# Kernel tuning notes

Measured on AMD Instinct MI355X. Metric: run time of the kernel, lower is better.

The kernel has to match this reference:

```python
import jax, jax.numpy as jnp
import numpy as np

N_NODES = 100000
N_EDGES = 1600000
VOCAB = 10000
HIDDEN = 128
EMB1 = 128
EMB2 = 128
L1 = 64
N_GRAPHS = 256


def setup_inputs() -> dict:
    key = jax.random.key(0)
    ks = jax.random.split(key, 16)
    inp = {
        "x": jax.random.randint(ks[0], (N_NODES,), 0, VOCAB, dtype=jnp.int32),
        "edge_index": jax.random.randint(ks[1], (2, N_EDGES), 0, N_NODES, dtype=jnp.int32),
        "edge_weight": jax.random.uniform(ks[2], (N_EDGES,), dtype=jnp.float32),
        "batch": jnp.sort(jax.random.randint(ks[3], (N_NODES,), 0, N_GRAPHS, dtype=jnp.int32)),
        # parameters
        "emb_w": jax.random.normal(ks[4], (VOCAB, HIDDEN), dtype=jnp.float32) * 0.5,
        "w1_rel": jax.random.normal(ks[5], (EMB1, HIDDEN), dtype=jnp.float32) * (HIDDEN ** -0.5),
        "b1_rel": jnp.zeros((EMB1,), dtype=jnp.float32),
        "w1_root": jax.random.normal(ks[6], (EMB1, HIDDEN), dtype=jnp.float32) * (HIDDEN ** -0.5),
        "w2_rel": jax.random.normal(ks[7], (EMB2, EMB1), dtype=jnp.float32) * (EMB1 ** -0.5),
        "b2_rel": jnp.zeros((EMB2,), dtype=jnp.float32),
        "w2_root": jax.random.normal(ks[8], (EMB2, EMB1), dtype=jnp.float32) * (EMB1 ** -0.5),
        "cls1_w": jax.random.normal(ks[9], (L1, EMB2), dtype=jnp.float32) * (EMB2 ** -0.5),
        "cls1_b": jnp.zeros((L1,), dtype=jnp.float32),
        "cls2_w": jax.random.normal(ks[10], (2, L1), dtype=jnp.float32) * (L1 ** -0.5),
        "cls2_b": jnp.zeros((2,), dtype=jnp.float32),
    }
    return inp


def _embedding_max_norm(emb_w, idx, max_norm=1.0):
    # torch Embedding(max_norm=1): looked-up rows are renormalized to norm <= 1
    rows = emb_w[idx]                                        # [N, H]
    norm = jnp.linalg.norm(rows, axis=-1, keepdims=True)
    scale = jnp.minimum(1.0, max_norm / (norm + 1e-7))
    return rows * scale


def _graph_conv(h, src, dst, ew, w_rel, b_rel, w_root):
    # PyG GraphConv: out = lin_rel(sum_{j->i} w_ji * x_j) + lin_root(x_i)
    msg = h[src] * ew[:, None]                               # [E, D] gather
    agg = jax.ops.segment_sum(msg, dst, num_segments=N_NODES)  # [N, D] scatter-add
    return agg @ w_rel.T + b_rel + h @ w_root.T


def reference(x, edge_index, edge_weight, batch, emb_w,
              w1_rel, b1_rel, w1_root, w2_rel, b2_rel, w2_root,
              cls1_w, cls1_b, cls2_w, cls2_b):
    src, dst = edge_index[0], edge_index[1]
    h = _embedding_max_norm(emb_w, x)                        # [N, HIDDEN]
    # dropout is identity in eval mode
    h = jax.nn.relu(_graph_conv(h, src, dst, edge_weight, w1_rel, b1_rel, w1_root))
    h = jax.nn.relu(_graph_conv(h, src, dst, edge_weight, w2_rel, b2_rel, w2_root))
    # global mean pool over graphs
    sums = jax.ops.segment_sum(h, batch, num_segments=N_GRAPHS)        # [G, EMB2]
    counts = jax.ops.segment_sum(jnp.ones((h.shape[0],), h.dtype), batch,
                                 num_segments=N_GRAPHS)
    pooled = sums / jnp.maximum(counts, 1.0)[:, None]
    z = jax.nn.relu(pooled @ cls1_w.T + cls1_b)
    z = z @ cls2_w.T + cls2_b
    return jax.nn.softmax(z, axis=1)                          # [G, 2]
```

## Files before the change

kernel.cpp:

```cpp
#include <hip/hip_runtime.h>
#include <stdint.h>

#define NN 100000
#define NE 1600000
#define NG 256
#define NB 196
#define CHUNK 4096
#define NCH 391
#define NGS 392

typedef __attribute__((ext_vector_type(8))) short bf16x8;
typedef __attribute__((ext_vector_type(4))) float f32x4;

__device__ inline uint32_t f2bf(float f){
    uint32_t u = __float_as_uint(f);
    return (u + 0x7FFFu + ((u >> 16) & 1u)) >> 16;
}
__device__ inline float bflo(uint32_t u){ return __uint_as_float(u << 16); }
__device__ inline float bfhi(uint32_t u){ return __uint_as_float(u & 0xFFFF0000u); }
__device__ inline float bf1(short s){ return __uint_as_float(((uint32_t)(uint16_t)s) << 16); }

__global__ __launch_bounds__(256) void k_pack(const float* __restrict__ w1rel, const float* __restrict__ w1root,
                                              const float* __restrict__ w2rel, const float* __restrict__ w2root,
                                              short* __restrict__ wf, int* __restrict__ bcnt){
    int id = blockIdx.x * 256 + threadIdx.x;
    if (id < NB) bcnt[id] = 0;
    int i = id & 7, lane = (id >> 3) & 63, ks = (id >> 9) & 3, j0 = (id >> 11) & 7, m = id >> 14;
    const float* W = (m == 0) ? w1rel : (m == 1) ? w1root : (m == 2) ? w2rel : w2root;
    int j = j0 * 16 + (lane & 15);
    int k = ks * 32 + (lane >> 4) * 8 + i;
    wf[id] = (short)f2bf(W[j * 128 + k]);
}

__global__ __launch_bounds__(256) void k_embed(const int* __restrict__ x,
                                               const float* __restrict__ emb,
                                               uint32_t* __restrict__ hout,
                                               const int* __restrict__ edst,
                                               int* __restrict__ bcnt,
                                               const int* __restrict__ batch,
                                               int* __restrict__ gstart){
    int bid = blockIdx.x;
    if (bid < NN / 4){
        int w = threadIdx.x >> 6, l = threadIdx.x & 63;
        int n = bid * 4 + w;
        int r = x[n];
        const float2* e2 = (const float2*)emb;
        float2 v = e2[(size_t)r * 64 + l];
        float ss = v.x * v.x + v.y * v.y;
        #pragma unroll
        for (int off = 32; off; off >>= 1) ss += __shfl_xor(ss, off, 64);
        float sc = fminf(1.f, 1.f / (sqrtf(ss) + 1e-7f));
        hout[(size_t)n * 64 + l] = f2bf(v.x * sc) | (f2bf(v.y * sc) << 16);
    } else if (bid < NN / 4 + NCH){
        __shared__ int lh[NB];
        int t = threadIdx.x;
        int c0 = (bid - NN / 4) * CHUNK;
        int cnt = min(CHUNK, NE - c0);
        if (t < NB) lh[t] = 0;
        __syncthreads();
        for (int i = t; i < cnt; i += 256) atomicAdd(&lh[edst[c0 + i] >> 9], 1);
        __syncthreads();
        if (t < NB && lh[t]) atomicAdd(&bcnt[t], lh[t]);
    } else {
        int i = (bid - NN / 4 - NCH) * 256 + threadIdx.x;
        if (i > NN) return;
        int bprev = (i == 0) ? -1 : batch[i - 1];
        int bcur  = (i == NN) ? NG : batch[i];
        for (int g = bprev + 1; g <= bcur; ++g) gstart[g] = i;
    }
}

__global__ __launch_bounds__(256) void k_bscan(const int* __restrict__ bcnt,
                                               int* __restrict__ bbase, int* __restrict__ bfill,
                                               int* __restrict__ ptrA){
    __shared__ int sc[256];
    int t = threadIdx.x;
    int v = (t < NB) ? bcnt[t] : 0;
    sc[t] = v; __syncthreads();
    for (int off = 1; off < 256; off <<= 1){
        int u = (t >= off) ? sc[t - off] : 0;
        __syncthreads();
        sc[t] += u;
        __syncthreads();
    }
    if (t < NB){ bbase[t] = sc[t] - v; bfill[t] = 0; }
    if (t == 0){ bbase[NB] = NE; ptrA[NN] = NE; }
}

__global__ __launch_bounds__(256) void k_bscatter(const int* __restrict__ esrc, const int* __restrict__ edst,
                                                  const float* __restrict__ ew,
                                                  const int* __restrict__ bbase, int* __restrict__ bfill,
                                                  uint2* __restrict__ cse2){
    __shared__ uint2 rec[CHUNK];
    __shared__ unsigned char slotb[CHUNK];
    __shared__ int hist[NB], start[NB], gbase[NB], sc[256];
    int t = threadIdx.x;
    int c0 = blockIdx.x * CHUNK;
    int cnt = min(CHUNK, NE - c0);
    if (t < NB) hist[t] = 0;
    __syncthreads();
    for (int i = t; i < cnt; i += 256) atomicAdd(&hist[edst[c0 + i] >> 9], 1);
    __syncthreads();
    int v = (t < NB) ? hist[t] : 0;
    sc[t] = v; __syncthreads();
    for (int off = 1; off < 256; off <<= 1){
        int u = (t >= off) ? sc[t - off] : 0;
        __syncthreads();
        sc[t] += u;
        __syncthreads();
    }
    if (t < NB){
        start[t] = sc[t] - v;
        if (v > 0) gbase[t] = bbase[t] + atomicAdd(&bfill[t], v);
    }
    __syncthreads();
    if (t < NB) hist[t] = 0;
    __syncthreads();
    for (int i = t; i < cnt; i += 256){
        int d = edst[c0 + i];
        int b = d >> 9;
        int slot = start[b] + atomicAdd(&hist[b], 1);
        rec[slot] = make_uint2((uint32_t)esrc[c0 + i] | ((uint32_t)(d & 511) << 23),
                               __float_as_uint(ew[c0 + i]));
        slotb[slot] = (unsigned char)b;
    }
    __syncthreads();
    for (int i = t; i < cnt; i += 256){
        int b = slotb[i];
        cse2[gbase[b] + (i - start[b])] = rec[i];
    }
}

__global__ __launch_bounds__(256) void k_bcsr(const uint2* __restrict__ cse2,
                                              const int* __restrict__ bbase,
                                              int* __restrict__ ptrA,
                                              uint2* __restrict__ cse){
    __shared__ int cnt[512], sc[512], st[512];
    int t = threadIdx.x;
    int b = blockIdx.x;
    int ebase = bbase[b], eend = bbase[b + 1];
    int nb = b << 9;
    cnt[t] = 0; cnt[t + 256] = 0;
    __syncthreads();
    for (int i = ebase + t; i < eend; i += 256){
        uint2 r = cse2[i];
        atomicAdd(&cnt[r.x >> 23], 1);
    }
    __syncthreads();
    sc[t] = cnt[t]; sc[t + 256] = cnt[t + 256];
    __syncthreads();
    for (int off = 1; off < 512; off <<= 1){
        int v0 = (t >= off) ? sc[t - off] : 0;
        int v1 = sc[t + 256 - off];
        __syncthreads();
        sc[t] += v0; sc[t + 256] += v1;
        __syncthreads();
    }
    st[t] = sc[t] - cnt[t];
    st[t + 256] = sc[t + 256] - cnt[t + 256];
    if (nb + t < NN)       ptrA[nb + t]       = ebase + st[t];
    if (nb + 256 + t < NN) ptrA[nb + 256 + t] = ebase + st[t + 256];
    cnt[t] = 0; cnt[t + 256] = 0;
    __syncthreads();
    for (int i = ebase + t; i < eend; i += 256){
        uint2 r = cse2[i];
        int dr = r.x >> 23;
        int pos = st[dr] + atomicAdd(&cnt[dr], 1);
        cse[ebase + pos] = make_uint2(r.x & 0x7FFFFFu, r.y);
    }
}

__global__ __launch_bounds__(256) void k_agg(const uint32_t* __restrict__ hin,
                                             uint32_t* __restrict__ aggo,
                                             const int* __restrict__ ptr,
                                             const uint2* __restrict__ cse){
    int w = threadIdx.x >> 6, l = threadIdx.x & 63;
    int h = l >> 5, c = l & 31;
    int n = blockIdx.x * 4 + w;
    int p0 = ptr[n], p1 = ptr[n + 1];
    const uint2* hin2 = (const uint2*)hin;
    float a0 = 0, a1 = 0, a2 = 0, a3 = 0;
    float b0 = 0, b1 = 0, b2 = 0, b3 = 0;
    int e = p0;
    for (; e + 8 <= p1; e += 8){
        uint2 rA0 = cse[e + 2 * h],     rB0 = cse[e + 2 * h + 1];
        uint2 rA1 = cse[e + 4 + 2 * h], rB1 = cse[e + 4 + 2 * h + 1];
        uint2 vA0 = hin2[(size_t)rA0.x * 32 + c];
        uint2 vB0 = hin2[(size_t)rB0.x * 32 + c];
        uint2 vA1 = hin2[(size_t)rA1.x * 32 + c];
        uint2 vB1 = hin2[(size_t)rB1.x * 32 + c];
        float wA0 = __uint_as_float(rA0.y), wB0 = __uint_as_float(rB0.y);
        float wA1 = __uint_as_float(rA1.y), wB1 = __uint_as_float(rB1.y);
        a0 += wA0 * bflo(vA0.x); a1 += wA0 * bfhi(vA0.x);
        a2 += wA0 * bflo(vA0.y); a3 += wA0 * bfhi(vA0.y);
        b0 += wB0 * bflo(vB0.x); b1 += wB0 * bfhi(vB0.x);
        b2 += wB0 * bflo(vB0.y); b3 += wB0 * bfhi(vB0.y);
        a0 += wA1 * bflo(vA1.x); a1 += wA1 * bfhi(vA1.x);
        a2 += wA1 * bflo(vA1.y); a3 += wA1 * bfhi(vA1.y);
        b0 += wB1 * bflo(vB1.x); b1 += wB1 * bfhi(vB1.x);
        b2 += wB1 * bflo(vB1.y); b3 += wB1 * bfhi(vB1.y);
    }
    for (; e + 4 <= p1; e += 4){
        uint2 rA = cse[e + 2 * h], rB = cse[e + 2 * h + 1];
        uint2 vA = hin2[(size_t)rA.x * 32 + c];
        uint2 vB = hin2[(size_t)rB.x * 32 + c];
        float wA = __uint_as_float(rA.y), wB = __uint_as_float(rB.y);
        a0 += wA * bflo(vA.x); a1 += wA * bfhi(vA.x);
        a2 += wA * bflo(vA.y); a3 += wA * bfhi(vA.y);
        b0 += wB * bflo(vB.x); b1 += wB * bfhi(vB.x);
        b2 += wB * bflo(vB.y); b3 += wB * bfhi(vB.y);
    }
    for (; e < p1; e += 2){
        int idx = e + h;
        bool act = idx < p1;
        uint2 r = act ? cse[idx] : make_uint2(0u, 0u);
        uint2 v = hin2[(size_t)r.x * 32 + c];
        float wt = act ? __uint_as_float(r.y) : 0.f;
        a0 += wt * bflo(v.x); a1 += wt * bfhi(v.x);
        a2 += wt * bflo(v.y); a3 += wt * bfhi(v.y);
    }
    a0 += b0; a1 += b1; a2 += b2; a3 += b3;
    a0 += __shfl_xor(a0, 32, 64);
    a1 += __shfl_xor(a1, 32, 64);
    a2 += __shfl_xor(a2, 32, 64);
    a3 += __shfl_xor(a3, 32, 64);
    if (h == 0){
        uint2 o;
        o.x = f2bf(a0) | (f2bf(a1) << 16);
        o.y = f2bf(a2) | (f2bf(a3) << 16);
        ((uint2*)aggo)[(size_t)n * 32 + c] = o;
    }
}

__global__ __launch_bounds__(256) void k_gemm(const short* __restrict__ hin,
                                              const short* __restrict__ agg,
                                              short* __restrict__ hout,
                                              const bf16x8* __restrict__ wrel,
                                              const bf16x8* __restrict__ wroot,
                                              const float* __restrict__ bias){
    int t = threadIdx.x, w = t >> 6, l = t & 63;
    int rbase = blockIdx.x * 128 + w * 32;
    int r0 = rbase + (l & 15);
    int rA0 = min(r0, NN - 1);
    int rA1 = min(r0 + 16, NN - 1);
    int kb = (l >> 4) * 8;

    bf16x8 aA[2][4], aH[2][4];
    const short* pa0 = agg + (size_t)rA0 * 128 + kb;
    const short* pa1 = agg + (size_t)rA1 * 128 + kb;
    const short* ph0 = hin + (size_t)rA0 * 128 + kb;
    const short* ph1 = hin + (size_t)rA1 * 128 + kb;
    #pragma unroll
    for (int ks = 0; ks < 4; ++ks){
        aA[0][ks] = *(const bf16x8*)(pa0 + ks * 32);
        aA[1][ks] = *(const bf16x8*)(pa1 + ks * 32);
        aH[0][ks] = *(const bf16x8*)(ph0 + ks * 32);
        aH[1][ks] = *(const bf16x8*)(ph1 + ks * 32);
    }

    for (int j0 = 0; j0 < 8; ++j0){
        f32x4 acc0 = {0.f, 0.f, 0.f, 0.f}, acc1 = {0.f, 0.f, 0.f, 0.f};
        #pragma unroll
        for (int ks = 0; ks < 4; ++ks){
            bf16x8 br = wrel [(j0 * 4 + ks) * 64 + l];
            bf16x8 bo = wroot[(j0 * 4 + ks) * 64 + l];
            acc0 = __builtin_amdgcn_mfma_f32_16x16x32_bf16(aA[0][ks], br, acc0, 0, 0, 0);
            acc0 = __builtin_amdgcn_mfma_f32_16x16x32_bf16(aH[0][ks], bo, acc0, 0, 0, 0);
            acc1 = __builtin_amdgcn_mfma_f32_16x16x32_bf16(aA[1][ks], br, acc1, 0, 0, 0);
            acc1 = __builtin_amdgcn_mfma_f32_16x16x32_bf16(aH[1][ks], bo, acc1, 0, 0, 0);
        }
        int col = j0 * 16 + (l & 15);
        float bv = bias[col];
        int rb = rbase + (l >> 4) * 4;
        #pragma unroll
        for (int r = 0; r < 4; ++r){
            int row = rb + r;
            if (row < NN){
                float v = fmaxf(acc0[r] + bv, 0.f);
                hout[(size_t)row * 128 + col] = (short)f2bf(v);
            }
            int row1 = rb + 16 + r;
            if (row1 < NN){
                float v = fmaxf(acc1[r] + bv, 0.f);
                hout[(size_t)row1 * 128 + col] = (short)f2bf(v);
            }
        }
    }
}

__global__ __launch_bounds__(128) void k_poolcls(const short* __restrict__ h,
                                                 const int* __restrict__ gstart,
                                                 const float* __restrict__ c1w, const float* __restrict__ c1b,
                                                 const float* __restrict__ c2w, const float* __restrict__ c2b,
                                                 float* __restrict__ out){
    __shared__ float pl[128];
    __shared__ float z[64];
    __shared__ float logits[2];
    int g = blockIdx.x, t = threadIdx.x;
    int s = gstart[g], e = gstart[g + 1];
    float a0 = 0, a1 = 0, a2 = 0, a3 = 0;
    int i = s;
    for (; i + 3 < e; i += 4){
        a0 += bf1(h[(size_t)i * 128 + t]);
        a1 += bf1(h[(size_t)(i + 1) * 128 + t]);
        a2 += bf1(h[(size_t)(i + 2) * 128 + t]);
        a3 += bf1(h[(size_t)(i + 3) * 128 + t]);
    }
    for (; i < e; ++i) a0 += bf1(h[(size_t)i * 128 + t]);
    float sum = (a0 + a1) + (a2 + a3);
    int cnt = e - s;
    pl[t] = sum / fmaxf((float)cnt, 1.f);
    __syncthreads();
    if (t < 64){
        float acc = c1b[t];
        #pragma unroll 4
        for (int k = 0; k < 128; ++k) acc += pl[k] * c1w[t * 128 + k];
        z[t] = fmaxf(acc, 0.f);
    }
    __syncthreads();
    if (t < 2){
        float a = c2b[t];
        for (int k = 0; k < 64; ++k) a += z[k] * c2w[t * 64 + k];
        logits[t] = a;
    }
    __syncthreads();
    if (t == 0){
        float m = fmaxf(logits[0], logits[1]);
        float e0 = expf(logits[0] - m), e1 = expf(logits[1] - m);
        float ss = e0 + e1;
        out[g * 2 + 0] = e0 / ss;
        out[g * 2 + 1] = e1 / ss;
    }
}

extern "C" void kernel_launch(void* const* d_in, const int* in_sizes, int n_in,
                              void* d_out, int out_size, void* d_ws, size_t ws_size,
                              hipStream_t stream) {
    const int*   x      = (const int*)  d_in[0];
    const int*   eidx   = (const int*)  d_in[1];
    const float* ew     = (const float*)d_in[2];
    const int*   batch  = (const int*)  d_in[3];
    const float* emb    = (const float*)d_in[4];
    const float* w1rel  = (const float*)d_in[5];
    const float* b1     = (const float*)d_in[6];
    const float* w1root = (const float*)d_in[7];
    const float* w2rel  = (const float*)d_in[8];
    const float* b2     = (const float*)d_in[9];
    const float* w2root = (const float*)d_in[10];
    const float* c1w    = (const float*)d_in[11];
    const float* c1b    = (const float*)d_in[12];
    const float* c2w    = (const float*)d_in[13];
    const float* c2b    = (const float*)d_in[14];
    float* out = (float*)d_out;

    const int N = NN;
    const int E = NE;

    char* p = (char*)d_ws;
    auto alloc = [&](size_t bytes) -> void* {
        void* r = (void*)p;
        p += (bytes + 255) & ~(size_t)255;
        return r;
    };
    uint32_t* hA   = (uint32_t*)alloc((size_t)N * 64 * 4);
    uint32_t* hB   = (uint32_t*)alloc((size_t)N * 64 * 4);
    uint32_t* agg  = (uint32_t*)alloc((size_t)N * 64 * 4);
    int*   ptrA   = (int*)  alloc((size_t)(N + 1) * 4);
    int*   bcnt   = (int*)  alloc(NB * 4);
    int*   bbase  = (int*)  alloc((NB + 1) * 4);
    int*   bfill  = (int*)  alloc(NB * 4);
    uint2* cse2   = (uint2*)alloc((size_t)E * 8);
    uint2* cse    = (uint2*)alloc((size_t)E * 8);
    int*   gstart = (int*)  alloc((NG + 1) * 4);
    short* wf     = (short*)alloc(4 * 16384 * 2);
    (void)alloc(65536);

    const bf16x8* wf1rel  = (const bf16x8*)(wf);
    const bf16x8* wf1root = (const bf16x8*)(wf + 16384);
    const bf16x8* wf2rel  = (const bf16x8*)(wf + 32768);
    const bf16x8* wf2root = (const bf16x8*)(wf + 49152);

    const int* esrc = eidx;
    const int* edst = eidx + E;

    k_pack <<<256, 256, 0, stream>>>(w1rel, w1root, w2rel, w2root, wf, bcnt);
    k_embed<<<N / 4 + NCH + NGS, 256, 0, stream>>>(x, emb, hA, edst, bcnt, batch, gstart);

    k_bscan   <<<1,   256, 0, stream>>>(bcnt, bbase, bfill, ptrA);
    k_bscatter<<<NCH, 256, 0, stream>>>(esrc, edst, ew, bbase, bfill, cse2);
    k_bcsr    <<<NB,  256, 0, stream>>>(cse2, bbase, ptrA, cse);

    int ngemm = (N + 127) / 128;
    k_agg <<<N / 4, 256, 0, stream>>>(hA, agg, ptrA, cse);
    k_gemm<<<ngemm, 256, 0, stream>>>((const short*)hA, (const short*)agg, (short*)hB,
                                      wf1rel, wf1root, b1);
    k_agg <<<N / 4, 256, 0, stream>>>(hB, agg, ptrA, cse);
    k_gemm<<<ngemm, 256, 0, stream>>>((const short*)hB, (const short*)agg, (short*)hA,
                                      wf2rel, wf2root, b2);

    k_poolcls<<<NG, 128, 0, stream>>>((const short*)hA, gstart, c1w, c1b, c2w, c2b, out);
}
```

Baseline: 377.0 us.

## Use 16-byte gathers with quarter-wave edges and finer dst buckets

The aggregation kernel now has 16 lanes per 256-byte row, each loading a uint4 (8 bf16 values), and 4 edges in flight per wave instead of 2. CSR entries store the precomputed byte offset of the source row, so address math is a single add. Destination buckets shrink from 512 to 256 nodes (391 buckets), which changes the packing bits and the per-bucket local sort. This raises bytes per gather instruction and memory-level parallelism, in exchange for a larger bucket histogram and a two-step 8-accumulator shuffle reduction.

```diff
diff --git a/kernel.cpp b/kernel.cpp
--- a/kernel.cpp
+++ b/kernel.cpp
@@ -4,7 +4,7 @@
 #define NN 100000
 #define NE 1600000
 #define NG 256
-#define NB 196
+#define NB 391
 #define CHUNK 4096
 #define NCH 391
 #define NGS 392
@@ -56,11 +56,13 @@
         int t = threadIdx.x;
         int c0 = (bid - NN / 4) * CHUNK;
         int cnt = min(CHUNK, NE - c0);
-        if (t < NB) lh[t] = 0;
-        __syncthreads();
-        for (int i = t; i < cnt; i += 256) atomicAdd(&lh[edst[c0 + i] >> 9], 1);
-        __syncthreads();
-        if (t < NB && lh[t]) atomicAdd(&bcnt[t], lh[t]);
+        lh[t] = 0;
+        if (t + 256 < NB) lh[t + 256] = 0;
+        __syncthreads();
+        for (int i = t; i < cnt; i += 256) atomicAdd(&lh[edst[c0 + i] >> 8], 1);
+        __syncthreads();
+        if (lh[t]) atomicAdd(&bcnt[t], lh[t]);
+        if (t + 256 < NB && lh[t + 256]) atomicAdd(&bcnt[t + 256], lh[t + 256]);
     } else {
         int i = (bid - NN / 4 - NCH) * 256 + threadIdx.x;
         if (i > NN) return;
@@ -73,17 +75,21 @@
 __global__ __launch_bounds__(256) void k_bscan(const int* __restrict__ bcnt,
                                                int* __restrict__ bbase, int* __restrict__ bfill,
                                                int* __restrict__ ptrA){
-    __shared__ int sc[256];
+    __shared__ int sc[512];
     int t = threadIdx.x;
-    int v = (t < NB) ? bcnt[t] : 0;
-    sc[t] = v; __syncthreads();
-    for (int off = 1; off < 256; off <<= 1){
-        int u = (t >= off) ? sc[t - off] : 0;
-        __syncthreads();
-        sc[t] += u;
-        __syncthreads();
-    }
-    if (t < NB){ bbase[t] = sc[t] - v; bfill[t] = 0; }
+    int v0 = (t < NB) ? bcnt[t] : 0;
+    int v1 = (t + 256 < NB) ? bcnt[t + 256] : 0;
+    sc[t] = v0; sc[t + 256] = v1;
+    __syncthreads();
+    for (int off = 1; off < 512; off <<= 1){
+        int u0 = (t >= off) ? sc[t - off] : 0;
+        int u1 = sc[t + 256 - off];
+        __syncthreads();
+        sc[t] += u0; sc[t + 256] += u1;
+        __syncthreads();
+    }
+    if (t < NB){ bbase[t] = sc[t] - v0; bfill[t] = 0; }
+    if (t + 256 < NB){ bbase[t + 256] = sc[t + 256] - v1; bfill[t + 256] = 0; }
     if (t == 0){ bbase[NB] = NE; ptrA[NN] = NE; }
 }
 
@@ -92,37 +98,39 @@
                                                   const int* __restrict__ bbase, int* __restrict__ bfill,
                                                   uint2* __restrict__ cse2){
     __shared__ uint2 rec[CHUNK];
-    __shared__ unsigned char slotb[CHUNK];
-    __shared__ int hist[NB], start[NB], gbase[NB], sc[256];
+    __shared__ unsigned short slotb[CHUNK];
+    __shared__ int hist[512], start[512], gbase[512], sc[512];
     int t = threadIdx.x;
     int c0 = blockIdx.x * CHUNK;
     int cnt = min(CHUNK, NE - c0);
-    if (t < NB) hist[t] = 0;
-    __syncthreads();
-    for (int i = t; i < cnt; i += 256) atomicAdd(&hist[edst[c0 + i] >> 9], 1);
-    __syncthreads();
-    int v = (t < NB) ? hist[t] : 0;
-    sc[t] = v; __syncthreads();
-    for (int off = 1; off < 256; off <<= 1){
-        int u = (t >= off) ? sc[t - off] : 0;
-        __syncthreads();
-        sc[t] += u;
-        __syncthreads();
-    }
-    if (t < NB){
-        start[t] = sc[t] - v;
-        if (v > 0) gbase[t] = bbase[t] + atomicAdd(&bfill[t], v);
-    }
-    __syncthreads();
-    if (t < NB) hist[t] = 0;
+    hist[t] = 0; hist[t + 256] = 0;
+    __syncthreads();
+    for (int i = t; i < cnt; i += 256) atomicAdd(&hist[edst[c0 + i] >> 8], 1);
+    __syncthreads();
+    int v0 = hist[t], v1 = hist[t + 256];
+    sc[t] = v0; sc[t + 256] = v1;
+    __syncthreads();
+    for (int off = 1; off < 512; off <<= 1){
+        int u0 = (t >= off) ? sc[t - off] : 0;
+        int u1 = sc[t + 256 - off];
+        __syncthreads();
+        sc[t] += u0; sc[t + 256] += u1;
+        __syncthreads();
+    }
+    start[t] = sc[t] - v0;
+    start[t + 256] = sc[t + 256] - v1;
+    if (t < NB && v0 > 0) gbase[t] = bbase[t] + atomicAdd(&bfill[t], v0);
+    if (t + 256 < NB && v1 > 0) gbase[t + 256] = bbase[t + 256] + atomicAdd(&bfill[t + 256], v1);
+    __syncthreads();
+    hist[t] = 0; hist[t + 256] = 0;
     __syncthreads();
     for (int i = t; i < cnt; i += 256){
         int d = edst[c0 + i];
-        int b = d >> 9;
+        int b = d >> 8;
         int slot = start[b] + atomicAdd(&hist[b], 1);
-        rec[slot] = make_uint2((uint32_t)esrc[c0 + i] | ((uint32_t)(d & 511) << 23),
+        rec[slot] = make_uint2((uint32_t)esrc[c0 + i] | ((uint32_t)(d & 255) << 20),
                                __float_as_uint(ew[c0 + i]));
-        slotb[slot] = (unsigned char)b;
+        slotb[slot] = (unsigned short)b;
     }
     __syncthreads();
     for (int i = t; i < cnt; i += 256){
@@ -135,100 +143,102 @@
                                               const int* __restrict__ bbase,
                                               int* __restrict__ ptrA,
                                               uint2* __restrict__ cse){
-    __shared__ int cnt[512], sc[512], st[512];
+    __shared__ int cnt[256], sc[256], st[256];
     int t = threadIdx.x;
     int b = blockIdx.x;
     int ebase = bbase[b], eend = bbase[b + 1];
-    int nb = b << 9;
-    cnt[t] = 0; cnt[t + 256] = 0;
+    int nb = b << 8;
+    cnt[t] = 0;
+    __syncthreads();
+    for (int i = ebase + t; i < eend; i += 256){
+        atomicAdd(&cnt[cse2[i].x >> 20], 1);
+    }
+    __syncthreads();
+    int v = cnt[t];
+    sc[t] = v;
+    __syncthreads();
+    for (int off = 1; off < 256; off <<= 1){
+        int u = (t >= off) ? sc[t - off] : 0;
+        __syncthreads();
+        sc[t] += u;
+        __syncthreads();
+    }
+    st[t] = sc[t] - v;
+    if (nb + t < NN) ptrA[nb + t] = ebase + st[t];
+    cnt[t] = 0;
     __syncthreads();
     for (int i = ebase + t; i < eend; i += 256){
         uint2 r = cse2[i];
-        atomicAdd(&cnt[r.x >> 23], 1);
-    }
-    __syncthreads();
-    sc[t] = cnt[t]; sc[t + 256] = cnt[t + 256];
-    __syncthreads();
-    for (int off = 1; off < 512; off <<= 1){
-        int v0 = (t >= off) ? sc[t - off] : 0;
-        int v1 = sc[t + 256 - off];
-        __syncthreads();
-        sc[t] += v0; sc[t + 256] += v1;
-        __syncthreads();
-    }
-    st[t] = sc[t] - cnt[t];
-    st[t + 256] = sc[t + 256] - cnt[t + 256];
-    if (nb + t < NN)       ptrA[nb + t]       = ebase + st[t];
-    if (nb + 256 + t < NN) ptrA[nb + 256 + t] = ebase + st[t + 256];
-    cnt[t] = 0; cnt[t + 256] = 0;
-    __syncthreads();
-    for (int i = ebase + t; i < eend; i += 256){
-        uint2 r = cse2[i];
-        int dr = r.x >> 23;
+        int dr = r.x >> 20;
         int pos = st[dr] + atomicAdd(&cnt[dr], 1);
-        cse[ebase + pos] = make_uint2(r.x & 0x7FFFFFu, r.y);
-    }
-}
+        cse[ebase + pos] = make_uint2((r.x & 0xFFFFFu) << 8, r.y);
+    }
+}
+
+#define ACC8(vv, ww) \
+    a0 += ww * bflo(vv.x); a1 += ww * bfhi(vv.x); \
+    a2 += ww * bflo(vv.y); a3 += ww * bfhi(vv.y); \
+    a4 += ww * bflo(vv.z); a5 += ww * bfhi(vv.z); \
+    a6 += ww * bflo(vv.w); a7 += ww * bfhi(vv.w);
 
 __global__ __launch_bounds__(256) void k_agg(const uint32_t* __restrict__ hin,
                                              uint32_t* __restrict__ aggo,
                                              const int* __restrict__ ptr,
                                              const uint2* __restrict__ cse){
     int w = threadIdx.x >> 6, l = threadIdx.x & 63;
-    int h = l >> 5, c = l & 31;
+    int q = l >> 4, c = l & 15;
     int n = blockIdx.x * 4 + w;
     int p0 = ptr[n], p1 = ptr[n + 1];
-    const uint2* hin2 = (const uint2*)hin;
-    float a0 = 0, a1 = 0, a2 = 0, a3 = 0;
-    float b0 = 0, b1 = 0, b2 = 0, b3 = 0;
+    const char* hb = (const char*)hin;
+    uint32_t coff = (uint32_t)(c << 4);
+    float a0 = 0, a1 = 0, a2 = 0, a3 = 0, a4 = 0, a5 = 0, a6 = 0, a7 = 0;
     int e = p0;
+    for (; e + 16 <= p1; e += 16){
+        uint2 r0 = cse[e + q], r1 = cse[e + 4 + q], r2 = cse[e + 8 + q], r3 = cse[e + 12 + q];
+        uint4 v0 = *(const uint4*)(hb + (r0.x + coff));
+        uint4 v1 = *(const uint4*)(hb + (r1.x + coff));
+        uint4 v2 = *(const uint4*)(hb + (r2.x + coff));
+        uint4 v3 = *(const uint4*)(hb + (r3.x + coff));
+        float w0 = __uint_as_float(r0.y), w1 = __uint_as_float(r1.y);
+        float w2 = __uint_as_float(r2.y), w3 = __uint_as_float(r3.y);
+        ACC8(v0, w0); ACC8(v1, w1); ACC8(v2, w2); ACC8(v3, w3);
+    }
     for (; e + 8 <= p1; e += 8){
-        uint2 rA0 = cse[e + 2 * h],     rB0 = cse[e + 2 * h + 1];
-        uint2 rA1 = cse[e + 4 + 2 * h], rB1 = cse[e + 4 + 2 * h + 1];
-        uint2 vA0 = hin2[(size_t)rA0.x * 32 + c];
-        uint2 vB0 = hin2[(size_t)rB0.x * 32 + c];
-        uint2 vA1 = hin2[(size_t)rA1.x * 32 + c];
-        uint2 vB1 = hin2[(size_t)rB1.x * 32 + c];
-        float wA0 = __uint_as_float(rA0.y), wB0 = __uint_as_float(rB0.y);
-        float wA1 = __uint_as_float(rA1.y), wB1 = __uint_as_float(rB1.y);
-        a0 += wA0 * bflo(vA0.x); a1 += wA0 * bfhi(vA0.x);
-        a2 += wA0 * bflo(vA0.y); a3 += wA0 * bfhi(vA0.y);
-        b0 += wB0 * bflo(vB0.x); b1 += wB0 * bfhi(vB0.x);
-        b2 += wB0 * bflo(vB0.y); b3 += wB0 * bfhi(vB0.y);
-        a0 += wA1 * bflo(vA1.x); a1 += wA1 * bfhi(vA1.x);
-        a2 += wA1 * bflo(vA1.y); a3 += wA1 * bfhi(vA1.y);
-        b0 += wB1 * bflo(vB1.x); b1 += wB1 * bfhi(vB1.x);
-        b2 += wB1 * bflo(vB1.y); b3 += wB1 * bfhi(vB1.y);
+        uint2 r0 = cse[e + q], r1 = cse[e + 4 + q];
+        uint4 v0 = *(const uint4*)(hb + (r0.x + coff));
+        uint4 v1 = *(const uint4*)(hb + (r1.x + coff));
+        float w0 = __uint_as_float(r0.y), w1 = __uint_as_float(r1.y);
+        ACC8(v0, w0); ACC8(v1, w1);
     }
     for (; e + 4 <= p1; e += 4){
-        uint2 rA = cse[e + 2 * h], rB = cse[e + 2 * h + 1];
-        uint2 vA = hin2[(size_t)rA.x * 32 + c];
-        uint2 vB = hin2[(size_t)rB.x * 32 + c];
-        float wA = __uint_as_float(rA.y), wB = __uint_as_float(rB.y);
-        a0 += wA * bflo(vA.x); a1 += wA * bfhi(vA.x);
-        a2 += wA * bflo(vA.y); a3 += wA * bfhi(vA.y);
-        b0 += wB * bflo(vB.x); b1 += wB * bfhi(vB.x);
-        b2 += wB * bflo(vB.y); b3 += wB * bfhi(vB.y);
-    }
-    for (; e < p1; e += 2){
-        int idx = e + h;
-        bool act = idx < p1;
-        uint2 r = act ? cse[idx] : make_uint2(0u, 0u);
-        uint2 v = hin2[(size_t)r.x * 32 + c];
-        float wt = act ? __uint_as_float(r.y) : 0.f;
-        a0 += wt * bflo(v.x); a1 += wt * bfhi(v.x);
-        a2 += wt * bflo(v.y); a3 += wt * bfhi(v.y);
-    }
-    a0 += b0; a1 += b1; a2 += b2; a3 += b3;
-    a0 += __shfl_xor(a0, 32, 64);
-    a1 += __shfl_xor(a1, 32, 64);
-    a2 += __shfl_xor(a2, 32, 64);
-    a3 += __shfl_xor(a3, 32, 64);
-    if (h == 0){
-        uint2 o;
+        uint2 r0 = cse[e + q];
+        uint4 v0 = *(const uint4*)(hb + (r0.x + coff));
+        float w0 = __uint_as_float(r0.y);
+        ACC8(v0, w0);
+    }
+    if (e < p1){
+        int idx = e + q;
+        int cidx = (idx < p1) ? idx : (p1 - 1);
+        uint2 r0 = cse[cidx];
+        uint4 v0 = *(const uint4*)(hb + (r0.x + coff));
+        float w0 = (idx < p1) ? __uint_as_float(r0.y) : 0.f;
+        ACC8(v0, w0);
+    }
+    a0 += __shfl_xor(a0, 16, 64); a0 += __shfl_xor(a0, 32, 64);
+    a1 += __shfl_xor(a1, 16, 64); a1 += __shfl_xor(a1, 32, 64);
+    a2 += __shfl_xor(a2, 16, 64); a2 += __shfl_xor(a2, 32, 64);
+    a3 += __shfl_xor(a3, 16, 64); a3 += __shfl_xor(a3, 32, 64);
+    a4 += __shfl_xor(a4, 16, 64); a4 += __shfl_xor(a4, 32, 64);
+    a5 += __shfl_xor(a5, 16, 64); a5 += __shfl_xor(a5, 32, 64);
+    a6 += __shfl_xor(a6, 16, 64); a6 += __shfl_xor(a6, 32, 64);
+    a7 += __shfl_xor(a7, 16, 64); a7 += __shfl_xor(a7, 32, 64);
+    if (q == 0){
+        uint4 o;
         o.x = f2bf(a0) | (f2bf(a1) << 16);
         o.y = f2bf(a2) | (f2bf(a3) << 16);
-        ((uint2*)aggo)[(size_t)n * 32 + c] = o;
+        o.z = f2bf(a4) | (f2bf(a5) << 16);
+        o.w = f2bf(a6) | (f2bf(a7) << 16);
+        *(uint4*)((char*)aggo + (size_t)n * 256 + coff) = o;
     }
 }
 
```

New measurement: 362.6 us. 1.04x faster.
